# Performance work log

Measured on AMD Instinct MI355X. Metric: run time of the kernel, lower is better.

Reference implementation:

```python
import jax, jax.numpy as jnp
import numpy as np

H, FFN, NH = 1024, 4096, 16
DK = H // NH
SCALE = DK ** -0.5


def _ln(x, g, b, eps=1e-5):
    m = jnp.mean(x, axis=-1, keepdims=True)
    v = jnp.var(x, axis=-1, keepdims=True)
    return (x - m) * jax.lax.rsqrt(v + eps) * g + b


def setup_inputs() -> dict:
    key = jax.random.key(0)
    ks = jax.random.split(key, 16)
    B, S = 4, 2048
    s = lambda fan: fan ** -0.5
    d = {
        "x": jax.random.normal(ks[0], (B, S, H), jnp.float32),
        "attn_bias": jax.random.normal(ks[1], (1, NH, S, S), jnp.float32),
        "ln1_g": jnp.ones((H,), jnp.float32),
        "ln1_b": jnp.zeros((H,), jnp.float32),
        "Wq": jax.random.normal(ks[2], (H, H), jnp.float32) * s(H),
        "bq": jnp.zeros((H,), jnp.float32),
        "Wk": jax.random.normal(ks[3], (H, H), jnp.float32) * s(H),
        "bk": jnp.zeros((H,), jnp.float32),
        "Wv": jax.random.normal(ks[4], (H, H), jnp.float32) * s(H),
        "bv": jnp.zeros((H,), jnp.float32),
        "Wo": jax.random.normal(ks[5], (H, H), jnp.float32) * s(H),
        "bo": jnp.zeros((H,), jnp.float32),
        "ln2_g": jnp.ones((H,), jnp.float32),
        "ln2_b": jnp.zeros((H,), jnp.float32),
        "W1": jax.random.normal(ks[6], (H, FFN), jnp.float32) * s(H),
        "b1": jnp.zeros((FFN,), jnp.float32),
        "W2": jax.random.normal(ks[7], (FFN, H), jnp.float32) * s(FFN),
        "b2": jnp.zeros((H,), jnp.float32),
    }
    return d


def reference(x, attn_bias, ln1_g, ln1_b, Wq, bq, Wk, bk, Wv, bv, Wo, bo,
              ln2_g, ln2_b, W1, b1, W2, b2):
    B, S, _ = x.shape
    y = _ln(x, ln1_g, ln1_b)
    q = (y @ Wq + bq).reshape(B, S, NH, DK)
    k = (y @ Wk + bk).reshape(B, S, NH, DK)
    v = (y @ Wv + bv).reshape(B, S, NH, DK)
    scores = jnp.einsum("bqhd,bkhd->bhqk", q * SCALE, k) + attn_bias
    A = jax.nn.softmax(scores, axis=-1)
    out = jnp.einsum("bhqk,bkhd->bqhd", A, v).reshape(B, S, H)
    x = x + (out @ Wo + bo)
    y = _ln(x, ln2_g, ln2_b)
    y = jax.nn.gelu(y @ W1 + b1, approximate=False) @ W2 + b2
    return x + y
```

## Files before the change

### kernel.cpp

```cpp
#include <hip/hip_runtime.h>

#define DEVINL __device__ __forceinline__

typedef __bf16 bf16x8 __attribute__((ext_vector_type(8)));
typedef float f32x4 __attribute__((ext_vector_type(4)));
typedef unsigned short u16x4 __attribute__((ext_vector_type(4)));

static constexpr int Bb = 4, S = 2048, H = 1024, NH = 16, DK = 64, FF = 4096;
static constexpr int Mrows = Bb * S;
static constexpr int QS = 3 * H;

DEVINL unsigned short f2bf(float f) {
    union { __bf16 b; unsigned short u; } r;
    r.b = (__bf16)f;
    return r.u;
}

DEVINL unsigned pack_bf2(float a, float b) {
    union { __bf16 h[2]; unsigned u; } r;
    r.h[0] = (__bf16)a; r.h[1] = (__bf16)b;
    return r.u;
}

DEVINL void gld16(const void* g, void* l) {
    auto gp = reinterpret_cast<const __attribute__((address_space(1))) unsigned*>(
        reinterpret_cast<unsigned long long>(g));
    auto lp = reinterpret_cast<__attribute__((address_space(3))) unsigned*>(
        (unsigned)reinterpret_cast<unsigned long long>(l));
    __builtin_amdgcn_global_load_lds(gp, lp, 16, 0, 0);
}

__global__ __launch_bounds__(256)
void wcvt(const float* __restrict__ in, unsigned short* __restrict__ out, int K, int N) {
    __shared__ float t[32][33];
    int n0 = blockIdx.x * 32, k0 = blockIdx.y * 32;
    int tx = threadIdx.x, ty = threadIdx.y;
#pragma unroll
    for (int i = 0; i < 32; i += 8) t[ty + i][tx] = in[(size_t)(k0 + ty + i) * N + n0 + tx];
    __syncthreads();
#pragma unroll
    for (int i = 0; i < 32; i += 8) out[(size_t)(n0 + ty + i) * K + k0 + tx] = f2bf(t[tx][ty + i]);
}

__global__ __launch_bounds__(256)
void catbias(const float* __restrict__ a, const float* __restrict__ b,
             const float* __restrict__ c, float* __restrict__ o) {
    int i = blockIdx.x * 256 + threadIdx.x;
    float v = (i < 1024) ? a[i] : (i < 2048 ? b[i - 1024] : c[i - 2048]);
    o[i] = v;
}

__global__ __launch_bounds__(256)
void ln_kernel(const float* __restrict__ x, const float* __restrict__ g,
               const float* __restrict__ be, unsigned short* __restrict__ y) {
    int row = blockIdx.x, tid = threadIdx.x;
    const float4 v = ((const float4*)(x + (size_t)row * H))[tid];
    float s = v.x + v.y + v.z + v.w;
    float ss = v.x * v.x + v.y * v.y + v.z * v.z + v.w * v.w;
#pragma unroll
    for (int m = 1; m < 64; m <<= 1) { s += __shfl_xor(s, m); ss += __shfl_xor(ss, m); }
    __shared__ float red[2][4];
    int lane = tid & 63, w = tid >> 6;
    if (lane == 0) { red[0][w] = s; red[1][w] = ss; }
    __syncthreads();
    s = red[0][0] + red[0][1] + red[0][2] + red[0][3];
    ss = red[1][0] + red[1][1] + red[1][2] + red[1][3];
    float mean = s * (1.f / H);
    float var = ss * (1.f / H) - mean * mean;
    float rstd = rsqrtf(var + 1e-5f);
    float4 gv = ((const float4*)g)[tid];
    float4 bv = ((const float4*)be)[tid];
    ushort4 o;
    o.x = f2bf((v.x - mean) * rstd * gv.x + bv.x);
    o.y = f2bf((v.y - mean) * rstd * gv.y + bv.y);
    o.z = f2bf((v.z - mean) * rstd * gv.z + bv.z);
    o.w = f2bf((v.w - mean) * rstd * gv.w + bv.w);
    ((ushort4*)(y + (size_t)row * H))[tid] = o;
}

template <int EPI>
__global__ __launch_bounds__(512, 2)
void gemm8p(const unsigned short* __restrict__ A, const unsigned short* __restrict__ Bt,
            const float* __restrict__ bias, void* __restrict__ outp, int N, int K) {
    __shared__ __align__(16) char lds[131072];
    const int tid = threadIdx.x, lane = tid & 63, w = tid >> 6;
    const int wm = w >> 2, wn = w & 3;
    const int fr = lane & 15, fq = lane >> 4;
    const int nwg = gridDim.x, id = blockIdx.x;
    const int swz = (id & 7) * (nwg >> 3) + (id >> 3);
    const int m0 = (swz & 31) * 256, n0 = (swz >> 5) * 256;

    int srow[2], scol[2];
#pragma unroll
    for (int l = 0; l < 2; ++l) {
        int idx = l * 512 + tid;
        srow[l] = idx >> 3;
        scol[l] = ((idx & 7) ^ (srow[l] & 7)) * 8;
    }
    const int NT = K >> 6;

    auto stage = [&](int ht, int buf, int kt) {
        const unsigned short* src = (ht < 2) ? A : Bt;
        const int hh = ht & 1;
        char* dst = lds + ((ht < 2 ? 0 : 65536) + (buf * 2 + hh) * 16384);
        const int rbase = ((ht < 2) ? m0 : n0) + hh * 128;
        const int kb = kt * 64;
#pragma unroll
        for (int l = 0; l < 2; ++l)
            gld16(src + (size_t)(rbase + srow[l]) * K + kb + scol[l],
                  dst + (size_t)(l * 512 + tid) * 16);
    };

    int oa[2];
#pragma unroll
    for (int ks = 0; ks < 2; ++ks)
        oa[ks] = fr * 128 + (((ks * 4 + fq) ^ (fr & 7)) & 7) * 16;
    const int aBase0 = wm * 16384;
    const int bBase0 = 65536 + (wn >> 1) * 16384 + (wn & 1) * 8192;

    f32x4 acc[8][4] = {};
    bf16x8 aF[4][2], bF[4][2];

    stage(0, 0, 0); stage(1, 0, 0); stage(2, 0, 0); stage(3, 0, 0);
    if (NT > 1) {
        stage(0, 1, 1);
        asm volatile("s_waitcnt vmcnt(2)" ::: "memory");
    } else {
        asm volatile("s_waitcnt vmcnt(0)" ::: "memory");
    }
    __builtin_amdgcn_s_barrier();

    int buf = 0;
    for (int t = 0; t < NT; ++t, buf ^= 1) {
        const char* Ar = lds + aBase0 + buf * 32768;
        const char* Br = lds + bBase0 + buf * 32768;

#pragma unroll
        for (int mb = 0; mb < 4; ++mb)
#pragma unroll
            for (int ks = 0; ks < 2; ++ks)
                aF[mb][ks] = *(const bf16x8*)(Ar + mb * 2048 + oa[ks]);
#pragma unroll
        for (int nb = 0; nb < 2; ++nb)
#pragma unroll
            for (int ks = 0; ks < 2; ++ks)
                bF[nb][ks] = *(const bf16x8*)(Br + nb * 2048 + oa[ks]);
        if (t + 1 < NT) stage(1, buf ^ 1, t + 1);
        __builtin_amdgcn_s_barrier();
        asm volatile("s_waitcnt lgkmcnt(0)" ::: "memory");
        __builtin_amdgcn_sched_barrier(0);
        __builtin_amdgcn_s_setprio(1);
#pragma unroll
        for (int mb = 0; mb < 4; ++mb)
#pragma unroll
            for (int nb = 0; nb < 2; ++nb)
#pragma unroll
                for (int ks = 0; ks < 2; ++ks)
                    acc[mb][nb] = __builtin_amdgcn_mfma_f32_16x16x32_bf16(aF[mb][ks], bF[nb][ks], acc[mb][nb], 0, 0, 0);
        __builtin_amdgcn_s_setprio(0);
        __builtin_amdgcn_s_barrier();

#pragma unroll
        for (int nb = 2; nb < 4; ++nb)
#pragma unroll
            for (int ks = 0; ks < 2; ++ks)
                bF[nb][ks] = *(const bf16x8*)(Br + nb * 2048 + oa[ks]);
        if (t + 1 < NT) stage(2, buf ^ 1, t + 1);
        __builtin_amdgcn_s_barrier();
        asm volatile("s_waitcnt lgkmcnt(0)" ::: "memory");
        __builtin_amdgcn_sched_barrier(0);
        __builtin_amdgcn_s_setprio(1);
#pragma unroll
        for (int mb = 0; mb < 4; ++mb)
#pragma unroll
            for (int nb = 2; nb < 4; ++nb)
#pragma unroll
                for (int ks = 0; ks < 2; ++ks)
                    acc[mb][nb] = __builtin_amdgcn_mfma_f32_16x16x32_bf16(aF[mb][ks], bF[nb][ks], acc[mb][nb], 0, 0, 0);
        __builtin_amdgcn_s_setprio(0);
        __builtin_amdgcn_s_barrier();

#pragma unroll
        for (int mb = 0; mb < 4; ++mb)
#pragma unroll
            for (int ks = 0; ks < 2; ++ks)
                aF[mb][ks] = *(const bf16x8*)(Ar + 8192 + mb * 2048 + oa[ks]);
        if (t + 1 < NT) stage(3, buf ^ 1, t + 1);
        __builtin_amdgcn_s_barrier();
        asm volatile("s_waitcnt lgkmcnt(0)" ::: "memory");
        __builtin_amdgcn_sched_barrier(0);
        __builtin_amdgcn_s_setprio(1);
#pragma unroll
        for (int mb = 0; mb < 4; ++mb)
#pragma unroll
            for (int nb = 0; nb < 2; ++nb)
#pragma unroll
                for (int ks = 0; ks < 2; ++ks)
                    acc[4 + mb][nb] = __builtin_amdgcn_mfma_f32_16x16x32_bf16(aF[mb][ks], bF[nb][ks], acc[4 + mb][nb], 0, 0, 0);
        __builtin_amdgcn_s_setprio(0);
        __builtin_amdgcn_s_barrier();

        if (t + 2 < NT) {
            stage(0, buf, t + 2);
            asm volatile("s_waitcnt vmcnt(2)" ::: "memory");
        } else if (t + 1 < NT) {
            asm volatile("s_waitcnt vmcnt(0)" ::: "memory");
        }
        __builtin_amdgcn_s_barrier();
        __builtin_amdgcn_s_setprio(1);
#pragma unroll
        for (int mb = 0; mb < 4; ++mb)
#pragma unroll
            for (int nb = 2; nb < 4; ++nb)
#pragma unroll
                for (int ks = 0; ks < 2; ++ks)
                    acc[4 + mb][nb] = __builtin_amdgcn_mfma_f32_16x16x32_bf16(aF[mb][ks], bF[nb][ks], acc[4 + mb][nb], 0, 0, 0);
        __builtin_amdgcn_s_setprio(0);
        __builtin_amdgcn_s_barrier();
    }

#pragma unroll
    for (int mb = 0; mb < 8; ++mb) {
        int row0 = m0 + wm * 128 + mb * 16 + fq * 4;
#pragma unroll
        for (int nb = 0; nb < 4; ++nb) {
            int col = n0 + wn * 64 + nb * 16 + fr;
            float bz = bias[col];
#pragma unroll
            for (int j = 0; j < 4; ++j) {
                float vv = acc[mb][nb][j] + bz;
                size_t idx = (size_t)(row0 + j) * N + col;
                if (EPI == 0) {
                    ((unsigned short*)outp)[idx] = f2bf(vv);
                } else {
                    float tg = 0.5f * vv * (1.f + erff(vv * 0.70710678118654752f));
                    ((unsigned short*)outp)[idx] = f2bf(tg);
                }
            }
        }
    }
}

template <int EPI>
__global__ __launch_bounds__(512, 2)
void gemm8p128(const unsigned short* __restrict__ A, const unsigned short* __restrict__ Bt,
               const float* __restrict__ bias, const float* __restrict__ resid,
               void* __restrict__ outp, int N, int K) {
    __shared__ __align__(16) char lds[98304];
    const int tid = threadIdx.x, lane = tid & 63, w = tid >> 6;
    const int wm = w >> 2, wn = w & 3;
    const int fr = lane & 15, fq = lane >> 4;
    const int nwg = gridDim.x, id = blockIdx.x;
    const int swz = (id & 7) * (nwg >> 3) + (id >> 3);
    const int m0 = (swz & 63) * 128, n0 = (swz >> 6) * 256;

    int srow[2], scol[2];
#pragma unroll
    for (int l = 0; l < 2; ++l) {
        int idx = l * 512 + tid;
        srow[l] = idx >> 3;
        scol[l] = ((idx & 7) ^ (srow[l] & 7)) * 8;
    }
    const int NT = K >> 6;

    auto stageA = [&](int buf, int kt) {
        char* dst = lds + buf * 16384;
#pragma unroll
        for (int l = 0; l < 2; ++l)
            gld16(A + (size_t)(m0 + srow[l]) * K + kt * 64 + scol[l],
                  dst + (size_t)(l * 512 + tid) * 16);
    };
    auto stageB = [&](int hh, int buf, int kt) {
        char* dst = lds + 32768 + buf * 32768 + hh * 16384;
#pragma unroll
        for (int l = 0; l < 2; ++l)
            gld16(Bt + (size_t)(n0 + hh * 128 + srow[l]) * K + kt * 64 + scol[l],
                  dst + (size_t)(l * 512 + tid) * 16);
    };

    int oa[2], ob[2];
#pragma unroll
    for (int ks = 0; ks < 2; ++ks) {
        oa[ks] = fr * 128 + (((ks * 4 + fq) ^ (fr & 7)) & 7) * 16;
        ob[ks] = fr * 128 + (((ks * 4 + fq) ^ (fr & 7)) & 7) * 16;
    }
    const int aWB = wm * 8192;
    const int bWB = (wn >> 1) * 16384 + (wn & 1) * 8192;

    f32x4 acc[4][4] = {};
    bf16x8 aF[2][2], bF[4][2];

    stageA(0, 0); stageB(0, 0, 0); stageB(1, 0, 0);
    if (NT > 1) {
        stageA(1, 1);
        asm volatile("s_waitcnt vmcnt(2)" ::: "memory");
    } else {
        asm volatile("s_waitcnt vmcnt(0)" ::: "memory");
    }
    __builtin_amdgcn_s_barrier();

    int buf = 0;
    for (int t = 0; t < NT; ++t, buf ^= 1) {
        const char* Ar = lds + buf * 16384 + aWB;
        const char* Br = lds + 32768 + buf * 32768 + bWB;

#pragma unroll
        for (int mb = 0; mb < 2; ++mb)
#pragma unroll
            for (int ks = 0; ks < 2; ++ks)
                aF[mb][ks] = *(const bf16x8*)(Ar + mb * 2048 + oa[ks]);
#pragma unroll
        for (int nb = 0; nb < 2; ++nb)
#pragma unroll
            for (int ks = 0; ks < 2; ++ks)
                bF[nb][ks] = *(const bf16x8*)(Br + nb * 2048 + ob[ks]);
        if (t + 1 < NT) stageB(0, buf ^ 1, t + 1);
        __builtin_amdgcn_s_barrier();
        asm volatile("s_waitcnt lgkmcnt(0)" ::: "memory");
        __builtin_amdgcn_sched_barrier(0);
        __builtin_amdgcn_s_setprio(1);
#pragma unroll
        for (int mb = 0; mb < 2; ++mb)
#pragma unroll
            for (int nb = 0; nb < 2; ++nb)
#pragma unroll
                for (int ks = 0; ks < 2; ++ks)
                    acc[mb][nb] = __builtin_amdgcn_mfma_f32_16x16x32_bf16(aF[mb][ks], bF[nb][ks], acc[mb][nb], 0, 0, 0);
        __builtin_amdgcn_s_setprio(0);
        __builtin_amdgcn_s_barrier();

#pragma unroll
        for (int nb = 2; nb < 4; ++nb)
#pragma unroll
            for (int ks = 0; ks < 2; ++ks)
                bF[nb][ks] = *(const bf16x8*)(Br + nb * 2048 + ob[ks]);
        if (t + 1 < NT) stageB(1, buf ^ 1, t + 1);
        __builtin_amdgcn_s_barrier();
        asm volatile("s_waitcnt lgkmcnt(0)" ::: "memory");
        __builtin_amdgcn_sched_barrier(0);
        __builtin_amdgcn_s_setprio(1);
#pragma unroll
        for (int mb = 0; mb < 2; ++mb)
#pragma unroll
            for (int nb = 2; nb < 4; ++nb)
#pragma unroll
                for (int ks = 0; ks < 2; ++ks)
                    acc[mb][nb] = __builtin_amdgcn_mfma_f32_16x16x32_bf16(aF[mb][ks], bF[nb][ks], acc[mb][nb], 0, 0, 0);
        __builtin_amdgcn_s_setprio(0);
        __builtin_amdgcn_s_barrier();

#pragma unroll
        for (int mb = 0; mb < 2; ++mb)
#pragma unroll
            for (int ks = 0; ks < 2; ++ks)
                aF[mb][ks] = *(const bf16x8*)(Ar + 4096 + mb * 2048 + oa[ks]);
        __builtin_amdgcn_s_barrier();
        asm volatile("s_waitcnt lgkmcnt(0)" ::: "memory");
        __builtin_amdgcn_sched_barrier(0);
        __builtin_amdgcn_s_setprio(1);
#pragma unroll
        for (int mb = 0; mb < 2; ++mb)
#pragma unroll
            for (int nb = 0; nb < 2; ++nb)
#pragma unroll
                for (int ks = 0; ks < 2; ++ks)
                    acc[2 + mb][nb] = __builtin_amdgcn_mfma_f32_16x16x32_bf16(aF[mb][ks], bF[nb][ks], acc[2 + mb][nb], 0, 0, 0);
        __builtin_amdgcn_s_setprio(0);
        __builtin_amdgcn_s_barrier();

        if (t + 2 < NT) {
            stageA(buf, t + 2);
            asm volatile("s_waitcnt vmcnt(2)" ::: "memory");
        } else if (t + 1 < NT) {
            asm volatile("s_waitcnt vmcnt(0)" ::: "memory");
        }
        __builtin_amdgcn_s_barrier();
        __builtin_amdgcn_s_setprio(1);
#pragma unroll
        for (int mb = 0; mb < 2; ++mb)
#pragma unroll
            for (int nb = 2; nb < 4; ++nb)
#pragma unroll
                for (int ks = 0; ks < 2; ++ks)
                    acc[2 + mb][nb] = __builtin_amdgcn_mfma_f32_16x16x32_bf16(aF[mb][ks], bF[nb][ks], acc[2 + mb][nb], 0, 0, 0);
        __builtin_amdgcn_s_setprio(0);
        __builtin_amdgcn_s_barrier();
    }

#pragma unroll
    for (int mb = 0; mb < 4; ++mb) {
        int row0 = m0 + wm * 64 + mb * 16 + fq * 4;
#pragma unroll
        for (int nb = 0; nb < 4; ++nb) {
            int col = n0 + wn * 64 + nb * 16 + fr;
            float bz = bias[col];
#pragma unroll
            for (int j = 0; j < 4; ++j) {
                size_t idx = (size_t)(row0 + j) * N + col;
                float vv = acc[mb][nb][j] + bz;
                if (EPI == 0) {
                    ((unsigned short*)outp)[idx] = f2bf(vv);
                } else {
                    ((float*)outp)[idx] = vv + resid[idx];
                }
            }
        }
    }
}

__global__ __launch_bounds__(512, 4)
void attn_kernel(const unsigned short* __restrict__ QKV, const float* __restrict__ bias,
                 unsigned short* __restrict__ O) {
    __shared__ __align__(16) unsigned short lK[2][4096];
    __shared__ __align__(16) unsigned short lV[2][4096];
    const int tid = threadIdx.x, lane = tid & 63, w = tid >> 6;
    const int fr = lane & 15, fq = lane >> 4;

    const int bid = blockIdx.x;
    const int slice = (bid >> 5) * 8 + (bid & 7);
    const int b = (bid >> 3) & 3;
    const int h = slice >> 4;
    const int q0 = (slice & 15) * 128;

    const size_t base = (size_t)b * S * QS + h * DK;
    const unsigned short* Qp = QKV + base;
    const unsigned short* Kp = QKV + base + H;
    const unsigned short* Vp = QKV + base + 2 * H;
    const size_t obase = (size_t)b * S * H + h * DK;

    bf16x8 aq[2];
    {
        const unsigned short* qp = Qp + (size_t)(q0 + w * 16 + fr) * QS + fq * 8;
        aq[0] = *(const bf16x8*)qp;
        aq[1] = *(const bf16x8*)(qp + 32);
    }

    const int chk = w * 64 + lane;
    const int rK = chk >> 3, cK = ((chk & 7) ^ (rK & 7)) * 8;
    int vk, vd;
    {
        int ch = chk;
        int dch = ch & 1, j = (ch >> 1) & 3, fqi = (ch >> 3) & 3, half = (ch >> 5) & 1,
            c = (ch >> 6) & 3, ks = (ch >> 8) & 1;
        vk = ks * 32 + half * 16 + fqi * 4 + j; vd = c * 16 + dch * 8;
    }

    f32x4 oacc[4] = {};
    float lrun = 0.f;
    const float* bias_q = bias + (size_t)h * S * S + (size_t)(q0 + w * 16 + fr) * S;

    const float SC = 0.18033688f;
    const float BL = 1.44269504f;
    const float CC = -23.08312065f;

    auto stage = [&](int buf, int k0) {
        gld16(Kp + (size_t)(k0 + rK) * QS + cK, &lK[buf][w * 512]);
        gld16(Vp + (size_t)(k0 + vk) * QS + vd, &lV[buf][w * 512]);
    };

    stage(0, 0);
    int cur = 0;
    for (int kt = 0; kt < S / 64; ++kt) {
        const int k0 = kt * 64;
        __syncthreads();
        if (kt + 1 < S / 64) stage(cur ^ 1, k0 + 64);

        float4 bv4[4];
#pragma unroll
        for (int c = 0; c < 4; ++c)
            bv4[c] = *(const float4*)(bias_q + k0 + c * 16 + fq * 4);

        f32x4 sacc[4] = {};
        __builtin_amdgcn_s_setprio(1);
#pragma unroll
        for (int c = 0; c < 4; ++c) {
            int row = c * 16 + fr;
#pragma unroll
            for (int dh = 0; dh < 2; ++dh) {
                bf16x8 bk = *(const bf16x8*)((char*)lK[cur] +
                    ((row * 128 + dh * 64 + fq * 16) ^ ((row & 7) << 4)));
                sacc[c] = __builtin_amdgcn_mfma_f32_16x16x32_bf16(bk, aq[dh], sacc[c], 0, 0, 0);
            }
        }
        __builtin_amdgcn_s_setprio(0);

        float p[4][4];
#pragma unroll
        for (int c = 0; c < 4; ++c) {
            float b0 = fmaf(bv4[c].x, BL, CC);
            float b1 = fmaf(bv4[c].y, BL, CC);
            float b2 = fmaf(bv4[c].z, BL, CC);
            float b3 = fmaf(bv4[c].w, BL, CC);
            p[c][0] = exp2f(fmaf(sacc[c][0], SC, b0));
            p[c][1] = exp2f(fmaf(sacc[c][1], SC, b1));
            p[c][2] = exp2f(fmaf(sacc[c][2], SC, b2));
            p[c][3] = exp2f(fmaf(sacc[c][3], SC, b3));
            lrun += p[c][0] + p[c][1] + p[c][2] + p[c][3];
        }

        union { unsigned u[4]; bf16x8 v; } pa0, pa1;
        pa0.u[0] = pack_bf2(p[0][0], p[0][1]);
        pa0.u[1] = pack_bf2(p[0][2], p[0][3]);
        pa0.u[2] = pack_bf2(p[1][0], p[1][1]);
        pa0.u[3] = pack_bf2(p[1][2], p[1][3]);
        pa1.u[0] = pack_bf2(p[2][0], p[2][1]);
        pa1.u[1] = pack_bf2(p[2][2], p[2][3]);
        pa1.u[2] = pack_bf2(p[3][0], p[3][1]);
        pa1.u[3] = pack_bf2(p[3][2], p[3][3]);

        u16x4 ra0[4], rb0[4], ra1[4], rb1[4];
        {
            const char* v0 = (const char*)lV[cur];
            const char* v1 = (const char*)lV[cur] + 4096;
#pragma unroll
            for (int c = 0; c < 4; ++c) {
                unsigned ad = (unsigned)(unsigned long long)(v0 + c * 1024) + lane * 8;
                asm volatile("ds_read_b64_tr_b16 %0, %1" : "=&v"(ra0[c]) : "v"(ad));
                asm volatile("ds_read_b64_tr_b16 %0, %1 offset:512" : "=&v"(rb0[c]) : "v"(ad));
            }
#pragma unroll
            for (int c = 0; c < 4; ++c) {
                unsigned ad = (unsigned)(unsigned long long)(v1 + c * 1024) + lane * 8;
                asm volatile("ds_read_b64_tr_b16 %0, %1" : "=&v"(ra1[c]) : "v"(ad));
                asm volatile("ds_read_b64_tr_b16 %0, %1 offset:512" : "=&v"(rb1[c]) : "v"(ad));
            }
        }
        asm volatile("s_waitcnt lgkmcnt(8)" ::: "memory");
        __builtin_amdgcn_sched_barrier(0);
        __builtin_amdgcn_s_setprio(1);
#pragma unroll
        for (int c = 0; c < 4; ++c) {
            union { u16x4 h2[2]; bf16x8 v8; } u;
            u.h2[0] = ra0[c]; u.h2[1] = rb0[c];
            oacc[c] = __builtin_amdgcn_mfma_f32_16x16x32_bf16(pa0.v, u.v8, oacc[c], 0, 0, 0);
        }
        __builtin_amdgcn_s_setprio(0);
        asm volatile("s_waitcnt lgkmcnt(0)" ::: "memory");
        __builtin_amdgcn_sched_barrier(0);
        __builtin_amdgcn_s_setprio(1);
#pragma unroll
        for (int c = 0; c < 4; ++c) {
            union { u16x4 h2[2]; bf16x8 v8; } u;
            u.h2[0] = ra1[c]; u.h2[1] = rb1[c];
            oacc[c] = __builtin_amdgcn_mfma_f32_16x16x32_bf16(pa1.v, u.v8, oacc[c], 0, 0, 0);
        }
        __builtin_amdgcn_s_setprio(0);
        cur ^= 1;
    }

    lrun += __shfl_xor(lrun, 16);
    lrun += __shfl_xor(lrun, 32);
    float linv = 1.f / lrun;
    float lo[4];
#pragma unroll
    for (int j = 0; j < 4; ++j) lo[j] = __shfl(linv, fq * 4 + j);
#pragma unroll
    for (int c = 0; c < 4; ++c)
#pragma unroll
        for (int j = 0; j < 4; ++j) {
            int row = q0 + w * 16 + fq * 4 + j;
            int d = c * 16 + fr;
            O[obase + (size_t)row * H + d] = f2bf(oacc[c][j] * lo[j]);
        }
}

extern "C" void kernel_launch(void* const* d_in, const int* in_sizes, int n_in,
                              void* d_out, int out_size, void* d_ws, size_t ws_size,
                              hipStream_t stream) {
    const float* x    = (const float*)d_in[0];
    const float* ab   = (const float*)d_in[1];
    const float* ln1g = (const float*)d_in[2];
    const float* ln1b = (const float*)d_in[3];
    const float* Wq   = (const float*)d_in[4];
    const float* bq   = (const float*)d_in[5];
    const float* Wk   = (const float*)d_in[6];
    const float* bk   = (const float*)d_in[7];
    const float* Wv   = (const float*)d_in[8];
    const float* bv   = (const float*)d_in[9];
    const float* Wo   = (const float*)d_in[10];
    const float* bo   = (const float*)d_in[11];
    const float* ln2g = (const float*)d_in[12];
    const float* ln2b = (const float*)d_in[13];
    const float* W1   = (const float*)d_in[14];
    const float* b1   = (const float*)d_in[15];
    const float* W2   = (const float*)d_in[16];
    const float* b2   = (const float*)d_in[17];

    char* ws = (char*)d_ws;
    size_t off = 0;
    auto alloc = [&](size_t bytes) -> void* {
        void* p = ws + off;
        off += (bytes + 255) & ~(size_t)255;
        return p;
    };
    unsigned short* Wqt = (unsigned short*)alloc((size_t)H * H * 2);
    unsigned short* Wkt = (unsigned short*)alloc((size_t)H * H * 2);
    unsigned short* Wvt = (unsigned short*)alloc((size_t)H * H * 2);
    unsigned short* Wot = (unsigned short*)alloc((size_t)H * H * 2);
    unsigned short* W1t = (unsigned short*)alloc((size_t)H * FF * 2);
    unsigned short* W2t = (unsigned short*)alloc((size_t)H * FF * 2);
    float* bqkv        = (float*)alloc((size_t)QS * 4);
    unsigned short* ybuf = (unsigned short*)alloc((size_t)Mrows * H * 2);
    unsigned short* qkvb = (unsigned short*)alloc((size_t)Mrows * QS * 2);
    unsigned short* ob = (unsigned short*)alloc((size_t)Mrows * H * 2);
    unsigned short* hb = (unsigned short*)alloc((size_t)Mrows * FF * 2);
    (void)ws_size; (void)in_sizes; (void)n_in; (void)out_size;
    (void)Wkt; (void)Wvt;

    dim3 tb(32, 8, 1);
    wcvt<<<dim3(H / 32, H / 32), tb, 0, stream>>>(Wq, Wqt, H, H);
    wcvt<<<dim3(H / 32, H / 32), tb, 0, stream>>>(Wk, Wkt, H, H);
    wcvt<<<dim3(H / 32, H / 32), tb, 0, stream>>>(Wv, Wvt, H, H);
    wcvt<<<dim3(H / 32, H / 32), tb, 0, stream>>>(Wo, Wot, H, H);
    wcvt<<<dim3(FF / 32, H / 32), tb, 0, stream>>>(W1, W1t, H, FF);
    wcvt<<<dim3(H / 32, FF / 32), tb, 0, stream>>>(W2, W2t, FF, H);
    catbias<<<QS / 256, 256, 0, stream>>>(bq, bk, bv, bqkv);

    ln_kernel<<<Mrows, 256, 0, stream>>>(x, ln1g, ln1b, ybuf);

    gemm8p128<0><<<dim3((Mrows / 128) * (QS / 256)), 512, 0, stream>>>(ybuf, Wqt, bqkv, nullptr, qkvb, QS, H);

    attn_kernel<<<dim3(Bb * NH * (S / 128)), 512, 0, stream>>>(qkvb, ab, ob);

    gemm8p128<2><<<dim3((Mrows / 128) * (H / 256)), 512, 0, stream>>>(ob, Wot, bo, x, d_out, H, H);

    ln_kernel<<<Mrows, 256, 0, stream>>>((const float*)d_out, ln2g, ln2b, ybuf);

    gemm8p<1><<<dim3((Mrows / 256) * (FF / 256)), 512, 0, stream>>>(ybuf, W1t, b1, hb, FF, H);

    gemm8p128<2><<<dim3((Mrows / 128) * (H / 256)), 512, 0, stream>>>(hb, W2t, b2, (const float*)d_out, d_out, H, FF);
}
```

Before: 549.1 us.

## Use 128x128 GEMM tiles for N=1024 projections and fuse weight conversions

```diff
diff --git a/kernel.cpp b/kernel.cpp
--- a/kernel.cpp
+++ b/kernel.cpp
@@ -31,9 +31,24 @@
 }
 
 __global__ __launch_bounds__(256)
-void wcvt(const float* __restrict__ in, unsigned short* __restrict__ out, int K, int N) {
+void wcvt_all(const float* __restrict__ Wq, const float* __restrict__ Wk,
+              const float* __restrict__ Wv, const float* __restrict__ Wo,
+              const float* __restrict__ W1, const float* __restrict__ W2,
+              unsigned short* __restrict__ Wqt, unsigned short* __restrict__ Wot,
+              unsigned short* __restrict__ W1t, unsigned short* __restrict__ W2t) {
+    int id = blockIdx.x;
+    const float* in; unsigned short* out; int K, N;
+    if (id < 3072) {
+        int which = id >> 10; id &= 1023;
+        in = which == 0 ? Wq : (which == 1 ? Wk : Wv);
+        out = Wqt + (size_t)which * H * H; K = H; N = H;
+    } else if (id < 4096) { in = Wo; out = Wot; K = H; N = H; id -= 3072; }
+    else if (id < 8192)   { in = W1; out = W1t; K = H; N = FF; id -= 4096; }
+    else                  { in = W2; out = W2t; K = FF; N = H; id -= 8192; }
+    const int nx = N / 32;
+    const int n0 = (id % nx) * 32, k0 = (id / nx) * 32;
+
     __shared__ float t[32][33];
-    int n0 = blockIdx.x * 32, k0 = blockIdx.y * 32;
     int tx = threadIdx.x, ty = threadIdx.y;
 #pragma unroll
     for (int i = 0; i < 32; i += 8) t[ty + i][tx] = in[(size_t)(k0 + ty + i) * N + n0 + tx];
@@ -278,12 +293,10 @@
                   dst + (size_t)(l * 512 + tid) * 16);
     };
 
-    int oa[2], ob[2];
-#pragma unroll
-    for (int ks = 0; ks < 2; ++ks) {
+    int oa[2];
+#pragma unroll
+    for (int ks = 0; ks < 2; ++ks)
         oa[ks] = fr * 128 + (((ks * 4 + fq) ^ (fr & 7)) & 7) * 16;
-        ob[ks] = fr * 128 + (((ks * 4 + fq) ^ (fr & 7)) & 7) * 16;
-    }
     const int aWB = wm * 8192;
     const int bWB = (wn >> 1) * 16384 + (wn & 1) * 8192;
 
@@ -313,7 +326,7 @@
         for (int nb = 0; nb < 2; ++nb)
 #pragma unroll
             for (int ks = 0; ks < 2; ++ks)
-                bF[nb][ks] = *(const bf16x8*)(Br + nb * 2048 + ob[ks]);
+                bF[nb][ks] = *(const bf16x8*)(Br + nb * 2048 + oa[ks]);
         if (t + 1 < NT) stageB(0, buf ^ 1, t + 1);
         __builtin_amdgcn_s_barrier();
         asm volatile("s_waitcnt lgkmcnt(0)" ::: "memory");
@@ -333,7 +346,7 @@
         for (int nb = 2; nb < 4; ++nb)
 #pragma unroll
             for (int ks = 0; ks < 2; ++ks)
-                bF[nb][ks] = *(const bf16x8*)(Br + nb * 2048 + ob[ks]);
+                bF[nb][ks] = *(const bf16x8*)(Br + nb * 2048 + oa[ks]);
         if (t + 1 < NT) stageB(1, buf ^ 1, t + 1);
         __builtin_amdgcn_s_barrier();
         asm volatile("s_waitcnt lgkmcnt(0)" ::: "memory");
@@ -390,6 +403,130 @@
 #pragma unroll
     for (int mb = 0; mb < 4; ++mb) {
         int row0 = m0 + wm * 64 + mb * 16 + fq * 4;
+#pragma unroll
+        for (int nb = 0; nb < 4; ++nb) {
+            int col = n0 + wn * 64 + nb * 16 + fr;
+            float bz = bias[col];
+#pragma unroll
+            for (int j = 0; j < 4; ++j) {
+                size_t idx = (size_t)(row0 + j) * N + col;
+                float vv = acc[mb][nb][j] + bz;
+                if (EPI == 0) {
+                    ((unsigned short*)outp)[idx] = f2bf(vv);
+                } else {
+                    ((float*)outp)[idx] = vv + resid[idx];
+                }
+            }
+        }
+    }
+}
+
+template <int EPI>
+__global__ __launch_bounds__(512, 4)
+void gemm128(const unsigned short* __restrict__ A, const unsigned short* __restrict__ Bt,
+             const float* __restrict__ bias, const float* __restrict__ resid,
+             void* __restrict__ outp, int N, int K) {
+    __shared__ __align__(16) char lds[65536];
+    const int tid = threadIdx.x, lane = tid & 63, w = tid >> 6;
+    const int wm = w >> 1, wn = w & 1;
+    const int fr = lane & 15, fq = lane >> 4;
+    const int nwg = gridDim.x, id = blockIdx.x;
+    const int swz = (id & 7) * (nwg >> 3) + (id >> 3);
+    const int m0 = (swz & 63) * 128, n0 = (swz >> 6) * 128;
+
+    int srow[2], scol[2];
+#pragma unroll
+    for (int l = 0; l < 2; ++l) {
+        int idx = l * 512 + tid;
+        srow[l] = idx >> 3;
+        scol[l] = ((idx & 7) ^ (srow[l] & 7)) * 8;
+    }
+    const int NT = K >> 6;
+
+    auto stageA = [&](int buf, int kt) {
+        char* dst = lds + buf * 16384;
+#pragma unroll
+        for (int l = 0; l < 2; ++l)
+            gld16(A + (size_t)(m0 + srow[l]) * K + kt * 64 + scol[l],
+                  dst + (size_t)(l * 512 + tid) * 16);
+    };
+    auto stageB = [&](int buf, int kt) {
+        char* dst = lds + 32768 + buf * 16384;
+#pragma unroll
+        for (int l = 0; l < 2; ++l)
+            gld16(Bt + (size_t)(n0 + srow[l]) * K + kt * 64 + scol[l],
+                  dst + (size_t)(l * 512 + tid) * 16);
+    };
+
+    int oa[2];
+#pragma unroll
+    for (int ks = 0; ks < 2; ++ks)
+        oa[ks] = fr * 128 + (((ks * 4 + fq) ^ (fr & 7)) & 7) * 16;
+    const int aWB = wm * 4096;
+    const int bWB = wn * 8192;
+
+    f32x4 acc[2][4] = {};
+    bf16x8 aF[2][2], bF[2][2];
+
+    stageA(0, 0); stageB(0, 0);
+    asm volatile("s_waitcnt vmcnt(0)" ::: "memory");
+    __builtin_amdgcn_s_barrier();
+
+    int buf = 0;
+    for (int t = 0; t < NT; ++t, buf ^= 1) {
+        const char* Ar = lds + buf * 16384 + aWB;
+        const char* Br = lds + 32768 + buf * 16384 + bWB;
+
+#pragma unroll
+        for (int mb = 0; mb < 2; ++mb)
+#pragma unroll
+            for (int ks = 0; ks < 2; ++ks)
+                aF[mb][ks] = *(const bf16x8*)(Ar + mb * 2048 + oa[ks]);
+#pragma unroll
+        for (int nb = 0; nb < 2; ++nb)
+#pragma unroll
+            for (int ks = 0; ks < 2; ++ks)
+                bF[nb][ks] = *(const bf16x8*)(Br + nb * 2048 + oa[ks]);
+        if (t + 1 < NT) stageA(buf ^ 1, t + 1);
+        __builtin_amdgcn_s_barrier();
+        asm volatile("s_waitcnt lgkmcnt(0)" ::: "memory");
+        __builtin_amdgcn_sched_barrier(0);
+        __builtin_amdgcn_s_setprio(1);
+#pragma unroll
+        for (int mb = 0; mb < 2; ++mb)
+#pragma unroll
+            for (int nb = 0; nb < 2; ++nb)
+#pragma unroll
+                for (int ks = 0; ks < 2; ++ks)
+                    acc[mb][nb] = __builtin_amdgcn_mfma_f32_16x16x32_bf16(aF[mb][ks], bF[nb][ks], acc[mb][nb], 0, 0, 0);
+        __builtin_amdgcn_s_setprio(0);
+        __builtin_amdgcn_s_barrier();
+
+#pragma unroll
+        for (int nb = 0; nb < 2; ++nb)
+#pragma unroll
+            for (int ks = 0; ks < 2; ++ks)
+                bF[nb][ks] = *(const bf16x8*)(Br + (2 + nb) * 2048 + oa[ks]);
+        if (t + 1 < NT) stageB(buf ^ 1, t + 1);
+        __builtin_amdgcn_s_barrier();
+        asm volatile("s_waitcnt lgkmcnt(0)" ::: "memory");
+        __builtin_amdgcn_sched_barrier(0);
+        __builtin_amdgcn_s_setprio(1);
+#pragma unroll
+        for (int mb = 0; mb < 2; ++mb)
+#pragma unroll
+            for (int nb = 0; nb < 2; ++nb)
+#pragma unroll
+                for (int ks = 0; ks < 2; ++ks)
+                    acc[mb][2 + nb] = __builtin_amdgcn_mfma_f32_16x16x32_bf16(aF[mb][ks], bF[nb][ks], acc[mb][2 + nb], 0, 0, 0);
+        __builtin_amdgcn_s_setprio(0);
+        if (t + 1 < NT) asm volatile("s_waitcnt vmcnt(0)" ::: "memory");
+        __builtin_amdgcn_s_barrier();
+    }
+
+#pragma unroll
+    for (int mb = 0; mb < 2; ++mb) {
+        int row0 = m0 + wm * 32 + mb * 16 + fq * 4;
 #pragma unroll
         for (int nb = 0; nb < 4; ++nb) {
             int col = n0 + wn * 64 + nb * 16 + fr;
@@ -608,12 +745,7 @@
     (void)Wkt; (void)Wvt;
 
     dim3 tb(32, 8, 1);
-    wcvt<<<dim3(H / 32, H / 32), tb, 0, stream>>>(Wq, Wqt, H, H);
-    wcvt<<<dim3(H / 32, H / 32), tb, 0, stream>>>(Wk, Wkt, H, H);
-    wcvt<<<dim3(H / 32, H / 32), tb, 0, stream>>>(Wv, Wvt, H, H);
-    wcvt<<<dim3(H / 32, H / 32), tb, 0, stream>>>(Wo, Wot, H, H);
-    wcvt<<<dim3(FF / 32, H / 32), tb, 0, stream>>>(W1, W1t, H, FF);
-    wcvt<<<dim3(H / 32, FF / 32), tb, 0, stream>>>(W2, W2t, FF, H);
+    wcvt_all<<<dim3(12288), tb, 0, stream>>>(Wq, Wk, Wv, Wo, W1, W2, Wqt, Wot, W1t, W2t);
     catbias<<<QS / 256, 256, 0, stream>>>(bq, bk, bv, bqkv);
 
     ln_kernel<<<Mrows, 256, 0, stream>>>(x, ln1g, ln1b, ybuf);
@@ -622,11 +754,11 @@
 
     attn_kernel<<<dim3(Bb * NH * (S / 128)), 512, 0, stream>>>(qkvb, ab, ob);
 
-    gemm8p128<2><<<dim3((Mrows / 128) * (H / 256)), 512, 0, stream>>>(ob, Wot, bo, x, d_out, H, H);
+    gemm128<2><<<dim3((Mrows / 128) * (H / 128)), 512, 0, stream>>>(ob, Wot, bo, x, d_out, H, H);
 
     ln_kernel<<<Mrows, 256, 0, stream>>>((const float*)d_out, ln2g, ln2b, ybuf);
 
     gemm8p<1><<<dim3((Mrows / 256) * (FF / 256)), 512, 0, stream>>>(ybuf, W1t, b1, hb, FF, H);
 
-    gemm8p128<2><<<dim3((Mrows / 128) * (H / 256)), 512, 0, stream>>>(hb, W2t, b2, (const float*)d_out, d_out, H, FF);
-}
+    gemm128<2><<<dim3((Mrows / 128) * (H / 128)), 512, 0, stream>>>(hb, W2t, b2, (const float*)d_out, d_out, H, FF);
+}
```

Result: slower. 562.2 us (+2.4%).

## Software-pipeline attention with triple-buffered K/V and fuse weight conversion launches

Applied to the files above, without the earlier changes.

```diff
diff --git a/kernel.cpp b/kernel.cpp
--- a/kernel.cpp
+++ b/kernel.cpp
@@ -31,9 +31,24 @@
 }
 
 __global__ __launch_bounds__(256)
-void wcvt(const float* __restrict__ in, unsigned short* __restrict__ out, int K, int N) {
+void wcvt_all(const float* __restrict__ Wq, const float* __restrict__ Wk,
+              const float* __restrict__ Wv, const float* __restrict__ Wo,
+              const float* __restrict__ W1, const float* __restrict__ W2,
+              unsigned short* __restrict__ Wqt, unsigned short* __restrict__ Wot,
+              unsigned short* __restrict__ W1t, unsigned short* __restrict__ W2t) {
+    int id = blockIdx.x;
+    const float* in; unsigned short* out; int K, N;
+    if (id < 3072) {
+        int which = id >> 10; id &= 1023;
+        in = which == 0 ? Wq : (which == 1 ? Wk : Wv);
+        out = Wqt + (size_t)which * H * H; K = H; N = H;
+    } else if (id < 4096) { in = Wo; out = Wot; K = H; N = H; id -= 3072; }
+    else if (id < 8192)   { in = W1; out = W1t; K = H; N = FF; id -= 4096; }
+    else                  { in = W2; out = W2t; K = FF; N = H; id -= 8192; }
+    const int nx = N / 32;
+    const int n0 = (id % nx) * 32, k0 = (id / nx) * 32;
+
     __shared__ float t[32][33];
-    int n0 = blockIdx.x * 32, k0 = blockIdx.y * 32;
     int tx = threadIdx.x, ty = threadIdx.y;
 #pragma unroll
     for (int i = 0; i < 32; i += 8) t[ty + i][tx] = in[(size_t)(k0 + ty + i) * N + n0 + tx];
@@ -278,12 +293,10 @@
                   dst + (size_t)(l * 512 + tid) * 16);
     };
 
-    int oa[2], ob[2];
-#pragma unroll
-    for (int ks = 0; ks < 2; ++ks) {
+    int oa[2];
+#pragma unroll
+    for (int ks = 0; ks < 2; ++ks)
         oa[ks] = fr * 128 + (((ks * 4 + fq) ^ (fr & 7)) & 7) * 16;
-        ob[ks] = fr * 128 + (((ks * 4 + fq) ^ (fr & 7)) & 7) * 16;
-    }
     const int aWB = wm * 8192;
     const int bWB = (wn >> 1) * 16384 + (wn & 1) * 8192;
 
@@ -313,7 +326,7 @@
         for (int nb = 0; nb < 2; ++nb)
 #pragma unroll
             for (int ks = 0; ks < 2; ++ks)
-                bF[nb][ks] = *(const bf16x8*)(Br + nb * 2048 + ob[ks]);
+                bF[nb][ks] = *(const bf16x8*)(Br + nb * 2048 + oa[ks]);
         if (t + 1 < NT) stageB(0, buf ^ 1, t + 1);
         __builtin_amdgcn_s_barrier();
         asm volatile("s_waitcnt lgkmcnt(0)" ::: "memory");
@@ -333,7 +346,7 @@
         for (int nb = 2; nb < 4; ++nb)
 #pragma unroll
             for (int ks = 0; ks < 2; ++ks)
-                bF[nb][ks] = *(const bf16x8*)(Br + nb * 2048 + ob[ks]);
+                bF[nb][ks] = *(const bf16x8*)(Br + nb * 2048 + oa[ks]);
         if (t + 1 < NT) stageB(1, buf ^ 1, t + 1);
         __builtin_amdgcn_s_barrier();
         asm volatile("s_waitcnt lgkmcnt(0)" ::: "memory");
@@ -411,8 +424,8 @@
 __global__ __launch_bounds__(512, 4)
 void attn_kernel(const unsigned short* __restrict__ QKV, const float* __restrict__ bias,
                  unsigned short* __restrict__ O) {
-    __shared__ __align__(16) unsigned short lK[2][4096];
-    __shared__ __align__(16) unsigned short lV[2][4096];
+    __shared__ __align__(16) unsigned short lK[3][4096];
+    __shared__ __align__(16) unsigned short lV[3][4096];
     const int tid = threadIdx.x, lane = tid & 63, w = tid >> 6;
     const int fr = lane & 15, fq = lane >> 4;
 
@@ -458,18 +471,18 @@
         gld16(Vp + (size_t)(k0 + vk) * QS + vd, &lV[buf][w * 512]);
     };
 
+    union pa_t { unsigned u[4]; bf16x8 v; };
+    pa_t pa0, pa1;
+
     stage(0, 0);
-    int cur = 0;
-    for (int kt = 0; kt < S / 64; ++kt) {
-        const int k0 = kt * 64;
-        __syncthreads();
-        if (kt + 1 < S / 64) stage(cur ^ 1, k0 + 64);
-
+    __syncthreads();
+    stage(1, 64);
+
+    {
         float4 bv4[4];
 #pragma unroll
         for (int c = 0; c < 4; ++c)
-            bv4[c] = *(const float4*)(bias_q + k0 + c * 16 + fq * 4);
-
+            bv4[c] = *(const float4*)(bias_q + c * 16 + fq * 4);
         f32x4 sacc[4] = {};
         __builtin_amdgcn_s_setprio(1);
 #pragma unroll
@@ -477,13 +490,12 @@
             int row = c * 16 + fr;
 #pragma unroll
             for (int dh = 0; dh < 2; ++dh) {
-                bf16x8 bk = *(const bf16x8*)((char*)lK[cur] +
+                bf16x8 bk = *(const bf16x8*)((char*)&lK[0][0] +
                     ((row * 128 + dh * 64 + fq * 16) ^ ((row & 7) << 4)));
                 sacc[c] = __builtin_amdgcn_mfma_f32_16x16x32_bf16(bk, aq[dh], sacc[c], 0, 0, 0);
             }
         }
         __builtin_amdgcn_s_setprio(0);
-
         float p[4][4];
 #pragma unroll
         for (int c = 0; c < 4; ++c) {
@@ -497,8 +509,6 @@
             p[c][3] = exp2f(fmaf(sacc[c][3], SC, b3));
             lrun += p[c][0] + p[c][1] + p[c][2] + p[c][3];
         }
-
-        union { unsigned u[4]; bf16x8 v; } pa0, pa1;
         pa0.u[0] = pack_bf2(p[0][0], p[0][1]);
         pa0.u[1] = pack_bf2(p[0][2], p[0][3]);
         pa0.u[2] = pack_bf2(p[1][0], p[1][1]);
@@ -507,11 +517,36 @@
         pa1.u[1] = pack_bf2(p[2][2], p[2][3]);
         pa1.u[2] = pack_bf2(p[3][0], p[3][1]);
         pa1.u[3] = pack_bf2(p[3][2], p[3][3]);
-
-        u16x4 ra0[4], rb0[4], ra1[4], rb1[4];
+    }
+
+    int bST = 2, bQK = 1, bPV = 0;
+    for (int kt = 1; kt < S / 64; ++kt) {
+        __syncthreads();
+        if (kt + 1 < S / 64) stage(bST, (kt + 1) * 64);
+
+        float4 bv4[4];
+#pragma unroll
+        for (int c = 0; c < 4; ++c)
+            bv4[c] = *(const float4*)(bias_q + kt * 64 + c * 16 + fq * 4);
+
+        f32x4 sacc[4] = {};
+        __builtin_amdgcn_s_setprio(1);
+#pragma unroll
+        for (int c = 0; c < 4; ++c) {
+            int row = c * 16 + fr;
+#pragma unroll
+            for (int dh = 0; dh < 2; ++dh) {
+                bf16x8 bk = *(const bf16x8*)((char*)&lK[bQK][0] +
+                    ((row * 128 + dh * 64 + fq * 16) ^ ((row & 7) << 4)));
+                sacc[c] = __builtin_amdgcn_mfma_f32_16x16x32_bf16(bk, aq[dh], sacc[c], 0, 0, 0);
+            }
+        }
+        __builtin_amdgcn_s_setprio(0);
+
         {
-            const char* v0 = (const char*)lV[cur];
-            const char* v1 = (const char*)lV[cur] + 4096;
+            const char* v0 = (const char*)&lV[bPV][0];
+            const char* v1 = v0 + 4096;
+            u16x4 ra0[4], rb0[4], ra1[4], rb1[4];
 #pragma unroll
             for (int c = 0; c < 4; ++c) {
                 unsigned ad = (unsigned)(unsigned long long)(v0 + c * 1024) + lane * 8;
@@ -524,8 +559,69 @@
                 asm volatile("ds_read_b64_tr_b16 %0, %1" : "=&v"(ra1[c]) : "v"(ad));
                 asm volatile("ds_read_b64_tr_b16 %0, %1 offset:512" : "=&v"(rb1[c]) : "v"(ad));
             }
-        }
-        asm volatile("s_waitcnt lgkmcnt(8)" ::: "memory");
+            asm volatile("s_waitcnt lgkmcnt(0)" ::: "memory");
+            __builtin_amdgcn_sched_barrier(0);
+            __builtin_amdgcn_s_setprio(1);
+#pragma unroll
+            for (int c = 0; c < 4; ++c) {
+                union { u16x4 h2[2]; bf16x8 v8; } u;
+                u.h2[0] = ra0[c]; u.h2[1] = rb0[c];
+                oacc[c] = __builtin_amdgcn_mfma_f32_16x16x32_bf16(pa0.v, u.v8, oacc[c], 0, 0, 0);
+            }
+#pragma unroll
+            for (int c = 0; c < 4; ++c) {
+                union { u16x4 h2[2]; bf16x8 v8; } u;
+                u.h2[0] = ra1[c]; u.h2[1] = rb1[c];
+                oacc[c] = __builtin_amdgcn_mfma_f32_16x16x32_bf16(pa1.v, u.v8, oacc[c], 0, 0, 0);
+            }
+            __builtin_amdgcn_s_setprio(0);
+            __builtin_amdgcn_sched_barrier(0);
+        }
+
+        {
+            float p[4][4];
+#pragma unroll
+            for (int c = 0; c < 4; ++c) {
+                float b0 = fmaf(bv4[c].x, BL, CC);
+                float b1 = fmaf(bv4[c].y, BL, CC);
+                float b2 = fmaf(bv4[c].z, BL, CC);
+                float b3 = fmaf(bv4[c].w, BL, CC);
+                p[c][0] = exp2f(fmaf(sacc[c][0], SC, b0));
+                p[c][1] = exp2f(fmaf(sacc[c][1], SC, b1));
+                p[c][2] = exp2f(fmaf(sacc[c][2], SC, b2));
+                p[c][3] = exp2f(fmaf(sacc[c][3], SC, b3));
+                lrun += p[c][0] + p[c][1] + p[c][2] + p[c][3];
+            }
+            pa0.u[0] = pack_bf2(p[0][0], p[0][1]);
+            pa0.u[1] = pack_bf2(p[0][2], p[0][3]);
+            pa0.u[2] = pack_bf2(p[1][0], p[1][1]);
+            pa0.u[3] = pack_bf2(p[1][2], p[1][3]);
+            pa1.u[0] = pack_bf2(p[2][0], p[2][1]);
+            pa1.u[1] = pack_bf2(p[2][2], p[2][3]);
+            pa1.u[2] = pack_bf2(p[3][0], p[3][1]);
+            pa1.u[3] = pack_bf2(p[3][2], p[3][3]);
+        }
+
+        bPV = bQK; bQK = bST; bST = (bST == 2) ? 0 : bST + 1;
+    }
+
+    {
+        const char* v0 = (const char*)&lV[bPV][0];
+        const char* v1 = v0 + 4096;
+        u16x4 ra0[4], rb0[4], ra1[4], rb1[4];
+#pragma unroll
+        for (int c = 0; c < 4; ++c) {
+            unsigned ad = (unsigned)(unsigned long long)(v0 + c * 1024) + lane * 8;
+            asm volatile("ds_read_b64_tr_b16 %0, %1" : "=&v"(ra0[c]) : "v"(ad));
+            asm volatile("ds_read_b64_tr_b16 %0, %1 offset:512" : "=&v"(rb0[c]) : "v"(ad));
+        }
+#pragma unroll
+        for (int c = 0; c < 4; ++c) {
+            unsigned ad = (unsigned)(unsigned long long)(v1 + c * 1024) + lane * 8;
+            asm volatile("ds_read_b64_tr_b16 %0, %1" : "=&v"(ra1[c]) : "v"(ad));
+            asm volatile("ds_read_b64_tr_b16 %0, %1 offset:512" : "=&v"(rb1[c]) : "v"(ad));
+        }
+        asm volatile("s_waitcnt lgkmcnt(0)" ::: "memory");
         __builtin_amdgcn_sched_barrier(0);
         __builtin_amdgcn_s_setprio(1);
 #pragma unroll
@@ -534,10 +630,6 @@
             u.h2[0] = ra0[c]; u.h2[1] = rb0[c];
             oacc[c] = __builtin_amdgcn_mfma_f32_16x16x32_bf16(pa0.v, u.v8, oacc[c], 0, 0, 0);
         }
-        __builtin_amdgcn_s_setprio(0);
-        asm volatile("s_waitcnt lgkmcnt(0)" ::: "memory");
-        __builtin_amdgcn_sched_barrier(0);
-        __builtin_amdgcn_s_setprio(1);
 #pragma unroll
         for (int c = 0; c < 4; ++c) {
             union { u16x4 h2[2]; bf16x8 v8; } u;
@@ -545,7 +637,6 @@
             oacc[c] = __builtin_amdgcn_mfma_f32_16x16x32_bf16(pa1.v, u.v8, oacc[c], 0, 0, 0);
         }
         __builtin_amdgcn_s_setprio(0);
-        cur ^= 1;
     }
 
     lrun += __shfl_xor(lrun, 16);
@@ -608,12 +699,7 @@
     (void)Wkt; (void)Wvt;
 
     dim3 tb(32, 8, 1);
-    wcvt<<<dim3(H / 32, H / 32), tb, 0, stream>>>(Wq, Wqt, H, H);
-    wcvt<<<dim3(H / 32, H / 32), tb, 0, stream>>>(Wk, Wkt, H, H);
-    wcvt<<<dim3(H / 32, H / 32), tb, 0, stream>>>(Wv, Wvt, H, H);
-    wcvt<<<dim3(H / 32, H / 32), tb, 0, stream>>>(Wo, Wot, H, H);
-    wcvt<<<dim3(FF / 32, H / 32), tb, 0, stream>>>(W1, W1t, H, FF);
-    wcvt<<<dim3(H / 32, FF / 32), tb, 0, stream>>>(W2, W2t, FF, H);
+    wcvt_all<<<dim3(12288), tb, 0, stream>>>(Wq, Wk, Wv, Wo, W1, W2, Wqt, Wot, W1t, W2t);
     catbias<<<QS / 256, 256, 0, stream>>>(bq, bk, bv, bqkv);
 
     ln_kernel<<<Mrows, 256, 0, stream>>>(x, ln1g, ln1b, ybuf);
```

New measurement: 516.3 us. 6.0% less time.
